# Kernel tuning notes

Measured on AMD Instinct MI355X. Metric: run time of the kernel, lower is better.

Reference implementation:

```python
import jax, jax.numpy as jnp
import numpy as np

D = 1024
H = 16
HD = D // H
EPS = 1e-5


def layer_norm(x, g, b):
    mu = jnp.mean(x, axis=-1, keepdims=True)
    var = jnp.var(x, axis=-1, keepdims=True)
    return (x - mu) * jax.lax.rsqrt(var + EPS) * g + b


def setup_inputs() -> dict:
    key = jax.random.key(0)
    ks = jax.random.split(key, 16)
    s = 0.02
    return {
        "x": jax.random.normal(ks[0], (2, 2048, D), jnp.float32),
        "ln1_g": jnp.ones((D,), jnp.float32),
        "ln1_b": jnp.zeros((D,), jnp.float32),
        "Wq": jax.random.normal(ks[1], (D, D), jnp.float32) * s,
        "bq": jnp.zeros((D,), jnp.float32),
        "Wk": jax.random.normal(ks[2], (D, D), jnp.float32) * s,
        "bk": jnp.zeros((D,), jnp.float32),
        "Wv": jax.random.normal(ks[3], (D, D), jnp.float32) * s,
        "bv": jnp.zeros((D,), jnp.float32),
        "Wo": jax.random.normal(ks[4], (D, D), jnp.float32) * s,
        "bo": jnp.zeros((D,), jnp.float32),
        "ln2_g": jnp.ones((D,), jnp.float32),
        "ln2_b": jnp.zeros((D,), jnp.float32),
        "W1": jax.random.normal(ks[5], (D, 4 * D), jnp.float32) * s,
        "b1": jnp.zeros((4 * D,), jnp.float32),
        "W2": jax.random.normal(ks[6], (4 * D, D), jnp.float32) * s,
        "b2": jnp.zeros((D,), jnp.float32),
    }


def reference(x, ln1_g, ln1_b, Wq, bq, Wk, bk, Wv, bv, Wo, bo, ln2_g, ln2_b, W1, b1, W2, b2):
    B, T, _ = x.shape
    # --- attention sub-block (pre-LN) ---
    h = layer_norm(x, ln1_g, ln1_b)
    q = (h @ Wq + bq).reshape(B, T, H, HD).transpose(0, 2, 1, 3)  # [B,H,T,hd]
    k = (h @ Wk + bk).reshape(B, T, H, HD).transpose(0, 2, 1, 3)
    v = (h @ Wv + bv).reshape(B, T, H, HD).transpose(0, 2, 1, 3)
    scores = jnp.einsum("bhqd,bhkd->bhqk", q, k)  # full O(T^2) scores as in source
    causal = jnp.tril(jnp.ones((T, T), bool))
    scores = jnp.where(causal, scores, -jnp.inf)
    w = jax.nn.softmax(scores / np.sqrt(HD), axis=-1)
    ctx = jnp.einsum("bhqk,bhkd->bhqd", w, v)
    ctx = ctx.transpose(0, 2, 1, 3).reshape(B, T, D)
    x = x + (ctx @ Wo + bo)
    # --- MLP sub-block (pre-LN) ---
    h = layer_norm(x, ln2_g, ln2_b)
    h = jax.nn.gelu(h @ W1 + b1, approximate=False)
    x = x + (h @ W2 + b2)
    return x
```

## Files before the change

### kernel.cpp

```cpp
#include <hip/hip_runtime.h>
#include <math.h>


typedef _Float16 half8 __attribute__((ext_vector_type(8)));
typedef _Float16 half4v __attribute__((ext_vector_type(4)));
typedef float floatx4 __attribute__((ext_vector_type(4)));

#define DMODEL 1024
#define SEQT   2048
#define NTOK   4096
#define NHEAD  16
#define HDIM   64

__device__ __forceinline__ void llds16(const _Float16* g, _Float16* l) {
  __builtin_amdgcn_global_load_lds(
      (const __attribute__((address_space(1))) void*)g,
      (__attribute__((address_space(3))) void*)l, 16, 0, 0);
}

__global__ __launch_bounds__(256) void wtrans_kernel(
    const float* __restrict__ Wq, const float* __restrict__ Wk,
    const float* __restrict__ Wv, const float* __restrict__ Wo,
    const float* __restrict__ W1, const float* __restrict__ W2,
    _Float16* __restrict__ wt_base) {
  __shared__ float tilebuf[32][33];
  int id = blockIdx.x;
  const float* src; _Float16* dst; int K, N, t;
  if (id < 4096) {
    int s = id >> 10;
    src = (s == 0) ? Wq : (s == 1) ? Wk : (s == 2) ? Wv : Wo;
    dst = wt_base + (size_t)s * (1024 * 1024);
    K = 1024; N = 1024; t = id & 1023;
  } else if (id < 8192) {
    src = W1; dst = wt_base + (size_t)4 * 1024 * 1024; K = 1024; N = 4096; t = id - 4096;
  } else {
    src = W2; dst = wt_base + (size_t)8 * 1024 * 1024; K = 4096; N = 1024; t = id - 8192;
  }
  int tilesN = N >> 5;
  int tk = t / tilesN, tn = t % tilesN;
  int c = threadIdx.x & 31, r0 = threadIdx.x >> 5;
#pragma unroll
  for (int i = 0; i < 4; ++i) {
    int r = r0 + i * 8;
    tilebuf[r][c] = src[(size_t)(tk * 32 + r) * N + tn * 32 + c];
  }
  __syncthreads();
#pragma unroll
  for (int i = 0; i < 4; ++i) {
    int r = r0 + i * 8;
    dst[(size_t)(tn * 32 + r) * K + tk * 32 + c] = (_Float16)tilebuf[c][r];
  }
}

__global__ __launch_bounds__(256) void ln_kernel(
    const float* __restrict__ x, const float* __restrict__ g,
    const float* __restrict__ b, _Float16* __restrict__ out) {
  int row = blockIdx.x;
  int t = threadIdx.x;
  const float4 xv = ((const float4*)(x + (size_t)row * DMODEL))[t];
  float s = xv.x + xv.y + xv.z + xv.w;
  float s2 = xv.x * xv.x + xv.y * xv.y + xv.z * xv.z + xv.w * xv.w;
#pragma unroll
  for (int off = 32; off; off >>= 1) {
    s += __shfl_down(s, off);
    s2 += __shfl_down(s2, off);
  }
  __shared__ float red[8];
  int wid = t >> 6;
  if ((t & 63) == 0) { red[wid] = s; red[wid + 4] = s2; }
  __syncthreads();
  s = red[0] + red[1] + red[2] + red[3];
  s2 = red[4] + red[5] + red[6] + red[7];
  float mu = s * (1.0f / DMODEL);
  float var = s2 * (1.0f / DMODEL) - mu * mu;
  float rstd = rsqrtf(var + 1e-5f);
  const float4 gv = ((const float4*)g)[t];
  const float4 bv = ((const float4*)b)[t];
  half4v o;
  o[0] = (_Float16)((xv.x - mu) * rstd * gv.x + bv.x);
  o[1] = (_Float16)((xv.y - mu) * rstd * gv.y + bv.y);
  o[2] = (_Float16)((xv.z - mu) * rstd * gv.z + bv.z);
  o[3] = (_Float16)((xv.w - mu) * rstd * gv.w + bv.w);
  *(half4v*)(out + (size_t)row * DMODEL + t * 4) = o;
}

template <int MODE>
__global__ __launch_bounds__(256) void gemm_kernel(
    const _Float16* __restrict__ A, const _Float16* __restrict__ Bt0, int K,
    const float* __restrict__ bias0, const float* __restrict__ bias1,
    const float* __restrict__ bias2, const float* __restrict__ res,
    float* __restrict__ outf, _Float16* __restrict__ outh) {
  __shared__ __align__(16) _Float16 As[2][128 * 32];
  __shared__ __align__(16) _Float16 Bs[2][128 * 32];
  const int tid = threadIdx.x;
  const int m0 = blockIdx.x * 128;
  const _Float16* Bt;
  const float* bias;
  _Float16* outh_sel = outh;
  int n0, sel = 0;
  if (MODE == 0) {
    sel = blockIdx.y >> 3;
    n0 = (blockIdx.y & 7) * 128;
    Bt = Bt0 + (size_t)sel * (1024 * 1024);
    bias = (sel == 0) ? bias0 : (sel == 1) ? bias1 : bias2;
    outh_sel = outh + (size_t)sel * ((size_t)NTOK * DMODEL);
  } else {
    n0 = blockIdx.y * 128;
    Bt = Bt0;
    bias = bias0;
  }
  int Keff = K, koff = 0;
  if (MODE == 3) { Keff = K >> 1; koff = blockIdx.z * Keff; }
  const int w = tid >> 6, lane = tid & 63;
  const int l15 = lane & 15, q8 = lane >> 4;
  const int wrow = (w >> 1) * 64;
  const int wcol = (w & 1) * 64;
  const int csw = (q8 ^ ((l15 >> 1) & 3)) * 8;

  const _Float16* gA[2]; const _Float16* gB[2]; int ldsc[2];
#pragma unroll
  for (int i = 0; i < 2; ++i) {
    int idx = i * 256 + w * 64 + lane;
    int m = idx >> 2;
    int kq = ((idx & 3) ^ ((m >> 1) & 3)) * 8;
    gA[i] = A + (size_t)(m0 + m) * K + koff + kq;
    gB[i] = Bt + (size_t)(n0 + m) * K + koff + kq;
    ldsc[i] = idx * 8;
  }

  auto stage = [&](int buf) {
#pragma unroll
    for (int i = 0; i < 2; ++i) {
      llds16(gA[i], &As[buf][ldsc[i]]);
      gA[i] += 32;
    }
#pragma unroll
    for (int i = 0; i < 2; ++i) {
      llds16(gB[i], &Bs[buf][ldsc[i]]);
      gB[i] += 32;
    }
  };

  floatx4 acc[4][4];
#pragma unroll
  for (int i = 0; i < 4; ++i)
#pragma unroll
    for (int j = 0; j < 4; ++j) acc[i][j] = (floatx4){0.f, 0.f, 0.f, 0.f};

  const int nk = Keff >> 5;
  stage(0);
  __syncthreads();
  for (int t = 0; t < nk; ++t) {
    const int buf = t & 1;
    if (t + 1 < nk) stage(buf ^ 1);
    half8 af[4], bf[4];
#pragma unroll
    for (int i = 0; i < 4; ++i)
      af[i] = *(const half8*)&As[buf][(wrow + i * 16 + l15) * 32 + csw];
#pragma unroll
    for (int j = 0; j < 4; ++j)
      bf[j] = *(const half8*)&Bs[buf][(wcol + j * 16 + l15) * 32 + csw];
#pragma unroll
    for (int i = 0; i < 4; ++i)
#pragma unroll
      for (int j = 0; j < 4; ++j)
        acc[i][j] = __builtin_amdgcn_mfma_f32_16x16x32_f16(af[i], bf[j], acc[i][j], 0, 0, 0);
    __syncthreads();
  }

#pragma unroll
  for (int i = 0; i < 4; ++i) {
    int rowb = m0 + wrow + i * 16 + q8 * 4;
#pragma unroll
    for (int j = 0; j < 4; ++j) {
      int col = n0 + wcol + j * 16 + l15;
      float bval = bias[col];
#pragma unroll
      for (int r = 0; r < 4; ++r) {
        int row = rowb + r;
        float v = acc[i][j][r];
        if (MODE == 0) {
          v += bval;
          int bb = row >> 11, tt = row & 2047;
          int hh = col >> 6, hd = col & 63;
          if (sel == 2)
            outh_sel[((size_t)(bb * NHEAD + hh) * HDIM + hd) * SEQT + tt] = (_Float16)v;
          else
            outh_sel[((size_t)(bb * NHEAD + hh) * SEQT + tt) * HDIM + hd] = (_Float16)v;
        } else if (MODE == 1) {
          v += bval + res[(size_t)row * 1024 + col];
          outf[(size_t)row * 1024 + col] = v;
        } else if (MODE == 2) {
          v += bval;
          float z = 1.5957691216f * v * (1.0f + 0.044715f * v * v);
          float gl = v / (1.0f + __expf(-z));
          outh[(size_t)row * 4096 + col] = (_Float16)gl;
        } else {
          if (blockIdx.z == 0) v += bval + res[(size_t)row * 1024 + col];
          unsafeAtomicAdd(outf + (size_t)row * 1024 + col, v);
        }
      }
    }
  }
}

__global__ __launch_bounds__(256) void attn_kernel(
    const _Float16* __restrict__ q, const _Float16* __restrict__ k,
    const _Float16* __restrict__ vt, _Float16* __restrict__ ctx) {
  __shared__ __align__(16) _Float16 Ks[2][64 * 64];
  __shared__ __align__(16) _Float16 Vs[2][64 * 64];
  __shared__ __align__(16) _Float16 Ps[64 * 72];
  __shared__ float Lpart[4][64];
  const int tid = threadIdx.x;
  const int w = tid >> 6, lane = tid & 63;
  const int l15 = lane & 15, q8 = lane >> 4;
  const int bh = blockIdx.y;
  const int pr = blockIdx.x;
  const size_t base = (size_t)bh * SEQT * HDIM;

  const _Float16* gk0[2]; const _Float16* gv0[2]; int ldsc[2];
#pragma unroll
  for (int i = 0; i < 2; ++i) {
    int c = i * 256 + w * 64 + lane;
    int r = c >> 3, gc = ((c & 7) ^ (r & 7)) * 8;
    gk0[i] = k + base + (size_t)r * HDIM + gc;
    gv0[i] = vt + base + (size_t)r * SEQT + gc;
    ldsc[i] = c * 8;
  }
  auto stage = [&](int kt, int buf) {
#pragma unroll
    for (int i = 0; i < 2; ++i) {
      llds16(gk0[i] + (size_t)kt * (64 * HDIM), &Ks[buf][ldsc[i]]);
      llds16(gv0[i] + kt * 64, &Vs[buf][ldsc[i]]);
    }
  };

  const int rswA = (l15 & 7);
  const int cs0 = (q8 ^ rswA) * 8;
  const int cs1 = ((4 + q8) ^ rswA) * 8;

  int s = 0;
  stage(0, 0);
  __syncthreads();
  for (int ph = 0; ph < 2; ++ph) {
    const int qtile = ph ? 31 - pr : pr;
    const int ntile = qtile + 1;
    half8 bq[4][2];
#pragma unroll
    for (int nt = 0; nt < 4; ++nt) {
      const half8* qp = (const half8*)(q + base + (size_t)(qtile * 64 + nt * 16 + l15) * HDIM);
      bq[nt][0] = qp[q8];
      bq[nt][1] = qp[4 + q8];
    }
    floatx4 acc[4];
#pragma unroll
    for (int j = 0; j < 4; ++j) acc[j] = (floatx4){0.f, 0.f, 0.f, 0.f};
    float lsum[4] = {0.f, 0.f, 0.f, 0.f};

    for (int jt = 0; jt < ntile; ++jt, ++s) {
      const int buf = s & 1;
      if (s + 1 < 33) {
        int sn = s + 1;
        int nkt = (sn <= pr) ? sn : sn - (pr + 1);
        stage(nkt, buf ^ 1);
      }
      half8 ak0 = *(const half8*)&Ks[buf][(w * 16 + l15) * 64 + cs0];
      half8 ak1 = *(const half8*)&Ks[buf][(w * 16 + l15) * 64 + cs1];
      floatx4 sv[4];
#pragma unroll
      for (int nt = 0; nt < 4; ++nt) {
        sv[nt] = __builtin_amdgcn_mfma_f32_16x16x32_f16(ak0, bq[nt][0],
                                                        (floatx4){0.f, 0.f, 0.f, 0.f}, 0, 0, 0);
        sv[nt] = __builtin_amdgcn_mfma_f32_16x16x32_f16(ak1, bq[nt][1], sv[nt], 0, 0, 0);
      }
      const bool diag = (jt == ntile - 1);
#pragma unroll
      for (int nt = 0; nt < 4; ++nt) {
        half4v phv;
#pragma unroll
        for (int r = 0; r < 4; ++r) {
          float p = __expf(sv[nt][r] * 0.125f);
          if (diag) {
            p = (w * 16 + q8 * 4 + r <= nt * 16 + l15) ? p : 0.f;
          }
          lsum[nt] += p;
          phv[r] = (_Float16)p;
        }
        *(half4v*)&Ps[(nt * 16 + l15) * 72 + w * 16 + q8 * 4] = phv;
      }
      __syncthreads();
      half8 ap0 = *(const half8*)&Ps[(w * 16 + l15) * 72 + q8 * 8];
      half8 ap1 = *(const half8*)&Ps[(w * 16 + l15) * 72 + 32 + q8 * 8];
#pragma unroll
      for (int ntd = 0; ntd < 4; ++ntd) {
        half8 bv0 = *(const half8*)&Vs[buf][(ntd * 16 + l15) * 64 + cs0];
        half8 bv1 = *(const half8*)&Vs[buf][(ntd * 16 + l15) * 64 + cs1];
        acc[ntd] = __builtin_amdgcn_mfma_f32_16x16x32_f16(ap0, bv0, acc[ntd], 0, 0, 0);
        acc[ntd] = __builtin_amdgcn_mfma_f32_16x16x32_f16(ap1, bv1, acc[ntd], 0, 0, 0);
      }
      __syncthreads();
    }

#pragma unroll
    for (int nt = 0; nt < 4; ++nt) {
      lsum[nt] += __shfl_xor(lsum[nt], 16);
      lsum[nt] += __shfl_xor(lsum[nt], 32);
      if (q8 == 0) Lpart[w][nt * 16 + l15] = lsum[nt];
    }
    __syncthreads();
    const int b = bh >> 4, h = bh & 15;
#pragma unroll
    for (int r = 0; r < 4; ++r) {
      int qr = w * 16 + q8 * 4 + r;
      float inv = 1.0f / (Lpart[0][qr] + Lpart[1][qr] + Lpart[2][qr] + Lpart[3][qr]);
      int tg = qtile * 64 + qr;
      _Float16* op = ctx + ((size_t)(b * SEQT + tg)) * DMODEL + h * HDIM;
#pragma unroll
      for (int ntd = 0; ntd < 4; ++ntd)
        op[ntd * 16 + l15] = (_Float16)(acc[ntd][r] * inv);
    }
  }
}

extern "C" void kernel_launch(void* const* d_in, const int* in_sizes, int n_in,
                              void* d_out, int out_size, void* d_ws, size_t ws_size,
                              hipStream_t stream) {
  (void)in_sizes; (void)n_in; (void)out_size; (void)ws_size;
  const float* x    = (const float*)d_in[0];
  const float* ln1g = (const float*)d_in[1];
  const float* ln1b = (const float*)d_in[2];
  const float* Wq   = (const float*)d_in[3];
  const float* bq   = (const float*)d_in[4];
  const float* Wk   = (const float*)d_in[5];
  const float* bk   = (const float*)d_in[6];
  const float* Wv   = (const float*)d_in[7];
  const float* bv   = (const float*)d_in[8];
  const float* Wo   = (const float*)d_in[9];
  const float* bo   = (const float*)d_in[10];
  const float* ln2g = (const float*)d_in[11];
  const float* ln2b = (const float*)d_in[12];
  const float* W1   = (const float*)d_in[13];
  const float* b1   = (const float*)d_in[14];
  const float* W2   = (const float*)d_in[15];
  const float* b2   = (const float*)d_in[16];
  float* out = (float*)d_out;

  char* ws = (char*)d_ws;
  _Float16* wt    = (_Float16*)(ws);
  _Float16* h16   = (_Float16*)(ws + ((size_t)24 << 20));
  _Float16* qkv   = (_Float16*)(ws + ((size_t)32 << 20));
  _Float16* ctx16 = (_Float16*)(ws + ((size_t)24 << 20));
  float*    x1    = (float*)   (ws + ((size_t)32 << 20));
  _Float16* h2    = (_Float16*)(ws + ((size_t)48 << 20));
  _Float16* mid   = (_Float16*)(ws + ((size_t)56 << 20));

  const size_t QKV1 = (size_t)NTOK * DMODEL;

  wtrans_kernel<<<12288, 256, 0, stream>>>(Wq, Wk, Wv, Wo, W1, W2, wt);
  ln_kernel<<<NTOK, 256, 0, stream>>>(x, ln1g, ln1b, h16);
  gemm_kernel<0><<<dim3(32, 24), 256, 0, stream>>>(
      h16, wt, 1024, bq, bk, bv, nullptr, nullptr, qkv);
  attn_kernel<<<dim3(16, 32), 256, 0, stream>>>(
      qkv, qkv + QKV1, qkv + 2 * QKV1, ctx16);
  gemm_kernel<1><<<dim3(32, 8), 256, 0, stream>>>(
      ctx16, wt + (size_t)3 * 1024 * 1024, 1024, bo, nullptr, nullptr, x, x1, nullptr);
  ln_kernel<<<NTOK, 256, 0, stream>>>(x1, ln2g, ln2b, h2);
  gemm_kernel<2><<<dim3(32, 32), 256, 0, stream>>>(
      h2, wt + (size_t)4 * 1024 * 1024, 1024, b1, nullptr, nullptr, nullptr, nullptr, mid);
  hipMemsetAsync(out, 0, (size_t)NTOK * DMODEL * sizeof(float), stream);
  gemm_kernel<3><<<dim3(32, 8, 2), 256, 0, stream>>>(
      mid, wt + (size_t)8 * 1024 * 1024, 4096, b2, nullptr, nullptr, x1, out, nullptr);
}
```

Measured before the change: 382.0 us.

## Fuse LN1 with weight transpose, add narrow-N GEMM, drop split-K atomics

LN1 and the weight transpose/convert now run in one launch, and the transpose uses 64x64 tiles with vectorized float4 loads and half8 stores. The out-projection and W2 GEMMs move to a new 128x64-tile kernel with a K-step of 64 and XOR-swizzled LDS. This removes the split-K atomics and the output memset. The V-transposed epilogue now writes half4 vectors, and one attention barrier is replaced by an explicit lgkmcnt wait plus s_barrier. These changes aim to cut launch count, atomic traffic and store inefficiency, at the cost of less parallelism per block for the K=4096 GEMM.

Result: faster. 353.3 us (-7.5%).

```diff
diff --git a/kernel.cpp b/kernel.cpp
--- a/kernel.cpp
+++ b/kernel.cpp
@@ -18,37 +18,77 @@
       (__attribute__((address_space(3))) void*)l, 16, 0, 0);
 }
 
-__global__ __launch_bounds__(256) void wtrans_kernel(
+__global__ __launch_bounds__(256) void prep_kernel(
+    const float* __restrict__ x, const float* __restrict__ g,
+    const float* __restrict__ b, _Float16* __restrict__ h16out,
     const float* __restrict__ Wq, const float* __restrict__ Wk,
     const float* __restrict__ Wv, const float* __restrict__ Wo,
     const float* __restrict__ W1, const float* __restrict__ W2,
     _Float16* __restrict__ wt_base) {
-  __shared__ float tilebuf[32][33];
-  int id = blockIdx.x;
+  const int t256 = threadIdx.x;
+  if (blockIdx.x < 4096) {
+    int row = blockIdx.x;
+    const float4 xv = ((const float4*)(x + (size_t)row * DMODEL))[t256];
+    float s = xv.x + xv.y + xv.z + xv.w;
+    float s2 = xv.x * xv.x + xv.y * xv.y + xv.z * xv.z + xv.w * xv.w;
+#pragma unroll
+    for (int off = 32; off; off >>= 1) {
+      s += __shfl_down(s, off);
+      s2 += __shfl_down(s2, off);
+    }
+    __shared__ float red[8];
+    int wid = t256 >> 6;
+    if ((t256 & 63) == 0) { red[wid] = s; red[wid + 4] = s2; }
+    __syncthreads();
+    s = red[0] + red[1] + red[2] + red[3];
+    s2 = red[4] + red[5] + red[6] + red[7];
+    float mu = s * (1.0f / DMODEL);
+    float var = s2 * (1.0f / DMODEL) - mu * mu;
+    float rstd = rsqrtf(var + 1e-5f);
+    const float4 gv = ((const float4*)g)[t256];
+    const float4 bv = ((const float4*)b)[t256];
+    half4v o;
+    o[0] = (_Float16)((xv.x - mu) * rstd * gv.x + bv.x);
+    o[1] = (_Float16)((xv.y - mu) * rstd * gv.y + bv.y);
+    o[2] = (_Float16)((xv.z - mu) * rstd * gv.z + bv.z);
+    o[3] = (_Float16)((xv.w - mu) * rstd * gv.w + bv.w);
+    *(half4v*)(h16out + (size_t)row * DMODEL + t256 * 4) = o;
+    return;
+  }
+  __shared__ float lb[64][65];
+  int id = blockIdx.x - 4096;
   const float* src; _Float16* dst; int K, N, t;
-  if (id < 4096) {
-    int s = id >> 10;
+  if (id < 1024) {
+    int s = id >> 8;
     src = (s == 0) ? Wq : (s == 1) ? Wk : (s == 2) ? Wv : Wo;
     dst = wt_base + (size_t)s * (1024 * 1024);
-    K = 1024; N = 1024; t = id & 1023;
-  } else if (id < 8192) {
-    src = W1; dst = wt_base + (size_t)4 * 1024 * 1024; K = 1024; N = 4096; t = id - 4096;
+    K = 1024; N = 1024; t = id & 255;
+  } else if (id < 2048) {
+    src = W1; dst = wt_base + (size_t)4 * 1024 * 1024; K = 1024; N = 4096; t = id - 1024;
   } else {
-    src = W2; dst = wt_base + (size_t)8 * 1024 * 1024; K = 4096; N = 1024; t = id - 8192;
-  }
-  int tilesN = N >> 5;
+    src = W2; dst = wt_base + (size_t)8 * 1024 * 1024; K = 4096; N = 1024; t = id - 2048;
+  }
+  int tilesN = N >> 6;
   int tk = t / tilesN, tn = t % tilesN;
-  int c = threadIdx.x & 31, r0 = threadIdx.x >> 5;
 #pragma unroll
   for (int i = 0; i < 4; ++i) {
-    int r = r0 + i * 8;
-    tilebuf[r][c] = src[(size_t)(tk * 32 + r) * N + tn * 32 + c];
+    int row = i * 16 + (t256 >> 4);
+    int c4 = (t256 & 15) * 4;
+    float4 v = *(const float4*)&src[(size_t)(tk * 64 + row) * N + tn * 64 + c4];
+    lb[row][c4] = v.x; lb[row][c4 + 1] = v.y;
+    lb[row][c4 + 2] = v.z; lb[row][c4 + 3] = v.w;
   }
   __syncthreads();
-#pragma unroll
-  for (int i = 0; i < 4; ++i) {
-    int r = r0 + i * 8;
-    dst[(size_t)(tn * 32 + r) * K + tk * 32 + c] = (_Float16)tilebuf[c][r];
+  {
+    int r = t256 >> 2, cb = t256 & 3;
+    half8 h0, h1;
+#pragma unroll
+    for (int kk = 0; kk < 8; ++kk) h0[kk] = (_Float16)lb[cb * 16 + kk][r];
+#pragma unroll
+    for (int kk = 0; kk < 8; ++kk) h1[kk] = (_Float16)lb[cb * 16 + 8 + kk][r];
+    _Float16* dp = dst + (size_t)(tn * 64 + r) * K + tk * 64 + cb * 16;
+    *(half8*)dp = h0;
+    *(half8*)(dp + 8) = h1;
   }
 }
 
@@ -88,8 +128,8 @@
 __global__ __launch_bounds__(256) void gemm_kernel(
     const _Float16* __restrict__ A, const _Float16* __restrict__ Bt0, int K,
     const float* __restrict__ bias0, const float* __restrict__ bias1,
-    const float* __restrict__ bias2, const float* __restrict__ res,
-    float* __restrict__ outf, _Float16* __restrict__ outh) {
+    const float* __restrict__ bias2,
+    _Float16* __restrict__ outh) {
   __shared__ __align__(16) _Float16 As[2][128 * 32];
   __shared__ __align__(16) _Float16 Bs[2][128 * 32];
   const int tid = threadIdx.x;
@@ -109,34 +149,35 @@
     Bt = Bt0;
     bias = bias0;
   }
-  int Keff = K, koff = 0;
-  if (MODE == 3) { Keff = K >> 1; koff = blockIdx.z * Keff; }
   const int w = tid >> 6, lane = tid & 63;
   const int l15 = lane & 15, q8 = lane >> 4;
   const int wrow = (w >> 1) * 64;
   const int wcol = (w & 1) * 64;
   const int csw = (q8 ^ ((l15 >> 1) & 3)) * 8;
 
-  const _Float16* gA[2]; const _Float16* gB[2]; int ldsc[2];
+  const _Float16* gA[2]; int ldsA[2];
+  const _Float16* gB[2]; int ldsB[2];
 #pragma unroll
   for (int i = 0; i < 2; ++i) {
-    int idx = i * 256 + w * 64 + lane;
+    int c0 = i * 256 + w * 64;
+    int idx = c0 + lane;
     int m = idx >> 2;
     int kq = ((idx & 3) ^ ((m >> 1) & 3)) * 8;
-    gA[i] = A + (size_t)(m0 + m) * K + koff + kq;
-    gB[i] = Bt + (size_t)(n0 + m) * K + koff + kq;
-    ldsc[i] = idx * 8;
+    gA[i] = A + (size_t)(m0 + m) * K + kq;
+    ldsA[i] = c0 * 8;
+    gB[i] = Bt + (size_t)(n0 + m) * K + kq;
+    ldsB[i] = c0 * 8;
   }
 
   auto stage = [&](int buf) {
 #pragma unroll
     for (int i = 0; i < 2; ++i) {
-      llds16(gA[i], &As[buf][ldsc[i]]);
+      llds16(gA[i], &As[buf][ldsA[i] + lane * 8]);
       gA[i] += 32;
     }
 #pragma unroll
     for (int i = 0; i < 2; ++i) {
-      llds16(gB[i], &Bs[buf][ldsc[i]]);
+      llds16(gB[i], &Bs[buf][ldsB[i] + lane * 8]);
       gB[i] += 32;
     }
   };
@@ -147,7 +188,7 @@
 #pragma unroll
     for (int j = 0; j < 4; ++j) acc[i][j] = (floatx4){0.f, 0.f, 0.f, 0.f};
 
-  const int nk = Keff >> 5;
+  const int nk = K >> 5;
   stage(0);
   __syncthreads();
   for (int t = 0; t < nk; ++t) {
@@ -175,30 +216,128 @@
     for (int j = 0; j < 4; ++j) {
       int col = n0 + wcol + j * 16 + l15;
       float bval = bias[col];
+      if (MODE == 0 && sel == 2) {
+        int bb = rowb >> 11, tt0 = rowb & 2047;
+        int hh = col >> 6, hd = col & 63;
+        half4v hv;
+#pragma unroll
+        for (int r = 0; r < 4; ++r) hv[r] = (_Float16)(acc[i][j][r] + bval);
+        *(half4v*)&outh_sel[((size_t)(bb * NHEAD + hh) * HDIM + hd) * SEQT + tt0] = hv;
+      } else {
+#pragma unroll
+        for (int r = 0; r < 4; ++r) {
+          int row = rowb + r;
+          float v = acc[i][j][r] + bval;
+          if (MODE == 0) {
+            int bb = row >> 11, tt = row & 2047;
+            int hh = col >> 6, hd = col & 63;
+            outh_sel[((size_t)(bb * NHEAD + hh) * SEQT + tt) * HDIM + hd] = (_Float16)v;
+          } else {
+            float z = 1.5957691216f * v * (1.0f + 0.044715f * v * v);
+            float gl = v / (1.0f + __expf(-z));
+            outh[(size_t)row * 4096 + col] = (_Float16)gl;
+          }
+        }
+      }
+    }
+  }
+}
+
+__global__ __launch_bounds__(256) void gemmw_kernel(
+    const _Float16* __restrict__ A, const _Float16* __restrict__ Bt, int K,
+    const float* __restrict__ bias, const float* __restrict__ res,
+    float* __restrict__ outf) {
+  __shared__ __align__(16) _Float16 As[2][128 * 64];
+  __shared__ __align__(16) _Float16 Bs[2][64 * 64];
+  const int tid = threadIdx.x;
+  const int m0 = blockIdx.x * 128;
+  const int n0 = blockIdx.y * 64;
+  const int w = tid >> 6, lane = tid & 63;
+  const int l15 = lane & 15, q8 = lane >> 4;
+  const int wrow = w * 32;
+
+  const _Float16* gA[4]; int la[4];
+  const _Float16* gB[2]; int lb2[2];
+#pragma unroll
+  for (int i = 0; i < 4; ++i) {
+    int c = i * 256 + tid;
+    int r = c >> 3, gc = ((c & 7) ^ (r & 7)) * 8;
+    gA[i] = A + (size_t)(m0 + r) * K + gc;
+    la[i] = c * 8;
+  }
+#pragma unroll
+  for (int i = 0; i < 2; ++i) {
+    int c = i * 256 + tid;
+    int r = c >> 3, gc = ((c & 7) ^ (r & 7)) * 8;
+    gB[i] = Bt + (size_t)(n0 + r) * K + gc;
+    lb2[i] = c * 8;
+  }
+  auto stage = [&](int buf) {
+#pragma unroll
+    for (int i = 0; i < 4; ++i) {
+      llds16(gA[i], &As[buf][la[i]]);
+      gA[i] += 64;
+    }
+#pragma unroll
+    for (int i = 0; i < 2; ++i) {
+      llds16(gB[i], &Bs[buf][lb2[i]]);
+      gB[i] += 64;
+    }
+  };
+
+  floatx4 acc[2][4];
+#pragma unroll
+  for (int i = 0; i < 2; ++i)
+#pragma unroll
+    for (int j = 0; j < 4; ++j) acc[i][j] = (floatx4){0.f, 0.f, 0.f, 0.f};
+
+  const int nk = K >> 6;
+  stage(0);
+  __syncthreads();
+  for (int t = 0; t < nk; ++t) {
+    const int buf = t & 1;
+    if (t + 1 < nk) stage(buf ^ 1);
+    half8 af[2][2], bf[4][2];
+#pragma unroll
+    for (int i = 0; i < 2; ++i) {
+      int rA = wrow + i * 16 + l15;
+#pragma unroll
+      for (int kh = 0; kh < 2; ++kh) {
+        int sl = ((kh * 4 + q8) ^ (rA & 7)) * 8;
+        af[i][kh] = *(const half8*)&As[buf][rA * 64 + sl];
+      }
+    }
+#pragma unroll
+    for (int j = 0; j < 4; ++j) {
+      int rB = j * 16 + l15;
+#pragma unroll
+      for (int kh = 0; kh < 2; ++kh) {
+        int sl = ((kh * 4 + q8) ^ (rB & 7)) * 8;
+        bf[j][kh] = *(const half8*)&Bs[buf][rB * 64 + sl];
+      }
+    }
+#pragma unroll
+    for (int i = 0; i < 2; ++i)
+#pragma unroll
+      for (int j = 0; j < 4; ++j) {
+        acc[i][j] = __builtin_amdgcn_mfma_f32_16x16x32_f16(af[i][0], bf[j][0], acc[i][j], 0, 0, 0);
+        acc[i][j] = __builtin_amdgcn_mfma_f32_16x16x32_f16(af[i][1], bf[j][1], acc[i][j], 0, 0, 0);
+      }
+    __syncthreads();
+  }
+
+#pragma unroll
+  for (int i = 0; i < 2; ++i) {
+    int rowb = m0 + wrow + i * 16 + q8 * 4;
+#pragma unroll
+    for (int j = 0; j < 4; ++j) {
+      int col = n0 + j * 16 + l15;
+      float bval = bias[col];
 #pragma unroll
       for (int r = 0; r < 4; ++r) {
         int row = rowb + r;
-        float v = acc[i][j][r];
-        if (MODE == 0) {
-          v += bval;
-          int bb = row >> 11, tt = row & 2047;
-          int hh = col >> 6, hd = col & 63;
-          if (sel == 2)
-            outh_sel[((size_t)(bb * NHEAD + hh) * HDIM + hd) * SEQT + tt] = (_Float16)v;
-          else
-            outh_sel[((size_t)(bb * NHEAD + hh) * SEQT + tt) * HDIM + hd] = (_Float16)v;
-        } else if (MODE == 1) {
-          v += bval + res[(size_t)row * 1024 + col];
-          outf[(size_t)row * 1024 + col] = v;
-        } else if (MODE == 2) {
-          v += bval;
-          float z = 1.5957691216f * v * (1.0f + 0.044715f * v * v);
-          float gl = v / (1.0f + __expf(-z));
-          outh[(size_t)row * 4096 + col] = (_Float16)gl;
-        } else {
-          if (blockIdx.z == 0) v += bval + res[(size_t)row * 1024 + col];
-          unsafeAtomicAdd(outf + (size_t)row * 1024 + col, v);
-        }
+        float v = acc[i][j][r] + bval + res[(size_t)row * 1024 + col];
+        outf[(size_t)row * 1024 + col] = v;
       }
     }
   }
@@ -288,7 +427,9 @@
         }
         *(half4v*)&Ps[(nt * 16 + l15) * 72 + w * 16 + q8 * 4] = phv;
       }
-      __syncthreads();
+      asm volatile("s_waitcnt lgkmcnt(0)" ::: "memory");
+      __builtin_amdgcn_s_barrier();
+      asm volatile("" ::: "memory");
       half8 ap0 = *(const half8*)&Ps[(w * 16 + l15) * 72 + q8 * 8];
       half8 ap1 = *(const half8*)&Ps[(w * 16 + l15) * 72 + 32 + q8 * 8];
 #pragma unroll
@@ -356,18 +497,17 @@
 
   const size_t QKV1 = (size_t)NTOK * DMODEL;
 
-  wtrans_kernel<<<12288, 256, 0, stream>>>(Wq, Wk, Wv, Wo, W1, W2, wt);
-  ln_kernel<<<NTOK, 256, 0, stream>>>(x, ln1g, ln1b, h16);
+  prep_kernel<<<7168, 256, 0, stream>>>(x, ln1g, ln1b, h16,
+                                        Wq, Wk, Wv, Wo, W1, W2, wt);
   gemm_kernel<0><<<dim3(32, 24), 256, 0, stream>>>(
-      h16, wt, 1024, bq, bk, bv, nullptr, nullptr, qkv);
+      h16, wt, 1024, bq, bk, bv, qkv);
   attn_kernel<<<dim3(16, 32), 256, 0, stream>>>(
       qkv, qkv + QKV1, qkv + 2 * QKV1, ctx16);
-  gemm_kernel<1><<<dim3(32, 8), 256, 0, stream>>>(
-      ctx16, wt + (size_t)3 * 1024 * 1024, 1024, bo, nullptr, nullptr, x, x1, nullptr);
+  gemmw_kernel<<<dim3(32, 16), 256, 0, stream>>>(
+      ctx16, wt + (size_t)3 * 1024 * 1024, 1024, bo, x, x1);
   ln_kernel<<<NTOK, 256, 0, stream>>>(x1, ln2g, ln2b, h2);
   gemm_kernel<2><<<dim3(32, 32), 256, 0, stream>>>(
-      h2, wt + (size_t)4 * 1024 * 1024, 1024, b1, nullptr, nullptr, nullptr, nullptr, mid);
-  hipMemsetAsync(out, 0, (size_t)NTOK * DMODEL * sizeof(float), stream);
-  gemm_kernel<3><<<dim3(32, 8, 2), 256, 0, stream>>>(
-      mid, wt + (size_t)8 * 1024 * 1024, 4096, b2, nullptr, nullptr, x1, out, nullptr);
-}
+      h2, wt + (size_t)4 * 1024 * 1024, 1024, b1, nullptr, nullptr, mid);
+  gemmw_kernel<<<dim3(32, 16), 256, 0, stream>>>(
+      mid, wt + (size_t)8 * 1024 * 1024, 4096, b2, x1, out);
+}
```
